# Kernel tuning notes

Hardware: AMD Instinct MI355X
Metric: run time of the kernel (lower is better)

Reference implementation:

```python
import jax, jax.numpy as jnp
import numpy as np

K = 5          # kernel_size
BETA = 15.0    # soft-max temperature
PAD = (K - 1) // 2  # fixed_padding with dilation=1: pad_beg = pad_end = 2


def setup_inputs() -> dict:
    key = jax.random.key(0)
    kx, kw = jax.random.split(key)
    x = jax.random.normal(kx, (16, 8, 256, 256), dtype=jnp.float32)
    weight = jax.random.normal(kw, (8, 8, K, K), dtype=jnp.float32) * 0.1
    return {"x": x, "weight": weight}


def reference(x, weight):
    """Morphological dilation2d with soft-max (logsumexp) reduction.

    Equivalent to: unfold(pad(x)) -> (B,1,C*K*K,L); add weight.view(O,-1);
    logsumexp(beta * .) / beta over the C*K*K axis; reshape to (B,O,H,W).
    Implemented as a streaming logsumexp over the K*K taps to avoid the
    huge unfold intermediate.
    """
    B, C, H, W = x.shape
    O = weight.shape[0]
    xp = jnp.pad(x, ((0, 0), (0, 0), (PAD, PAD), (PAD, PAD)))
    acc = None
    for ki in range(K):
        for kj in range(K):
            xs = xp[:, :, ki:ki + H, kj:kj + W]              # (B,C,H,W)
            w_tap = weight[:, :, ki, kj]                      # (O,C)
            # beta * (w + x), broadcast to (B,O,C,H,W)
            t = BETA * (xs[:, None, :, :, :] + w_tap[None, :, :, None, None])
            lse = jax.nn.logsumexp(t, axis=2)                 # (B,O,H,W)
            acc = lse if acc is None else jnp.logaddexp(acc, lse)
    return acc / BETA
```

## Files before the change

kernel.cpp:

```cpp
#include <hip/hip_runtime.h>
#include <hip/hip_bf16.h>
#include <math.h>

#define KW 5
#define BETA 15.0f
#define MSHIFT 3.0f
#define CIN 8
#define COUT 8
#define HH 256
#define WW 256
#define TW 64
#define THT 8
#define CWp 68
#define CHp 12

typedef float f32x4 __attribute__((ext_vector_type(4)));
typedef short s16x8 __attribute__((ext_vector_type(8)));

static __device__ __forceinline__ unsigned f2bf(float f) {
    unsigned u = __float_as_uint(f);
    return (u + 0x7FFFu + ((u >> 16) & 1u)) >> 16;
}

__global__ void build_afrag(const float* __restrict__ wgt,
                            s16x8* __restrict__ table) {
    int i = blockIdx.x * 64 + threadIdx.x;
    if (i >= 7 * 64) return;
    int g = i >> 6, lane = i & 63;
    int quad = lane >> 4, row = lane & 15;
    int tap = g * 4 + quad;
    s16x8 af;
    #pragma unroll
    for (int j = 0; j < CIN; ++j) {
        float v = 0.0f;
        if (tap < 25 && row < COUT)
            v = __expf(BETA * wgt[(row * CIN + j) * (KW * KW) + tap]);
        af[j] = (short)f2bf(v);
    }
    table[i] = af;
}

__global__ __launch_bounds__(256, 6) void morph_mfma(
    const float* __restrict__ x, const s16x8* __restrict__ table,
    float* __restrict__ out)
{
    __shared__ int4 exs[CHp * CWp];

    const int tid  = threadIdx.x;
    const int lane = tid & 63;
    const int wv   = tid >> 6;
    const int px   = lane & 15;
    const int quad = lane >> 4;

    const int lid = blockIdx.x;
    const int sw  = (lid & 7) * 256 + (lid >> 3);
    const int b   = sw >> 7;
    const int t   = sw & 127;
    const int h0  = (t >> 2) * THT;
    const int w0  = (t & 3) * TW;

    s16x8 afrag[7];
    int   toff[7];
    #pragma unroll
    for (int g = 0; g < 7; ++g) {
        afrag[g] = table[g * 64 + lane];
        int tap = g * 4 + quad;
        int tc  = tap < 25 ? tap : 24;
        toff[g] = (tc / KW) * CWp + (tc % KW);
    }

    for (int s = tid; s < CHp * CWp; s += 256) {
        int r = s / CWp, col = s - r * CWp;
        int gh = h0 + r - 2, gw = w0 + col - 2;
        bool ok = ((unsigned)gh < (unsigned)HH) & ((unsigned)gw < (unsigned)WW);
        unsigned pk[4];
        #pragma unroll
        for (int c2 = 0; c2 < 4; ++c2) {
            float v0 = 0.0f, v1 = 0.0f;
            if (ok) {
                v0 = x[((b * CIN + 2 * c2) * HH + gh) * WW + gw];
                v1 = x[((b * CIN + 2 * c2 + 1) * HH + gh) * WW + gw];
            }
            float2 e = make_float2(__expf(BETA * (v0 - MSHIFT)),
                                   __expf(BETA * (v1 - MSHIFT)));
            __hip_bfloat162 h2 = __float22bfloat162_rn(e);
            pk[c2] = *reinterpret_cast<unsigned*>(&h2);
        }
        int4 p; p.x = pk[0]; p.y = pk[1]; p.z = pk[2]; p.w = pk[3];
        exs[s] = p;
    }
    __syncthreads();

    const float inv_beta = 1.0f / BETA;
    #pragma unroll
    for (int hl = 0; hl < 2; ++hl) {
        const int hh = wv * 2 + hl;
        #pragma unroll
        for (int wb = 0; wb < 4; ++wb) {
            const int base = hh * CWp + wb * 16 + px;
            f32x4 acc0 = {0.0f, 0.0f, 0.0f, 0.0f};
            f32x4 acc1 = {0.0f, 0.0f, 0.0f, 0.0f};
            #pragma unroll
            for (int g = 0; g < 7; ++g) {
                s16x8 bfr = *(const s16x8*)&exs[base + toff[g]];
                if (g & 1)
                    acc1 = __builtin_amdgcn_mfma_f32_16x16x32_bf16(
                               afrag[g], bfr, acc1, 0, 0, 0);
                else
                    acc0 = __builtin_amdgcn_mfma_f32_16x16x32_bf16(
                               afrag[g], bfr, acc0, 0, 0, 0);
            }
            if (quad < 2) {
                #pragma unroll
                for (int r = 0; r < 4; ++r) {
                    int o = quad * 4 + r;
                    out[((b * COUT + o) * HH + h0 + hh) * WW + w0 + wb * 16 + px]
                        = MSHIFT + __logf(acc0[r] + acc1[r]) * inv_beta;
                }
            }
        }
    }
}

extern "C" void kernel_launch(void* const* d_in, const int* in_sizes, int n_in,
                              void* d_out, int out_size, void* d_ws, size_t ws_size,
                              hipStream_t stream) {
    const float* x   = (const float*)d_in[0];
    const float* wgt = (const float*)d_in[1];
    float* out  = (float*)d_out;
    s16x8* tab  = (s16x8*)d_ws;

    const int B = in_sizes[0] / (CIN * HH * WW);
    const int nblk = B * (HH / THT) * (WW / TW);

    build_afrag<<<7, 64, 0, stream>>>(wgt, tab);
    morph_mfma<<<nblk, 256, 0, stream>>>(x, tab, out);
}
```

Before: 99.42 us.

## Give each wave a private LDS halo tile and drop block barrier

Each of the four waves now stages its own 16x8 output tile plus halo (20x12 exp-transformed pixels) into a private LDS region and computes all 8 rows of it, so the block-wide __syncthreads is removed. This lets waves proceed independently, overlapping staging with MFMA work. The cost is redundant halo loads and exp computations between neighbouring waves and slightly more LDS per block.

```diff
diff --git a/kernel.cpp b/kernel.cpp
--- a/kernel.cpp
+++ b/kernel.cpp
@@ -9,10 +9,11 @@
 #define COUT 8
 #define HH 256
 #define WW 256
-#define TW 64
-#define THT 8
-#define CWp 68
-#define CHp 12
+#define TWW 16
+#define TWH 8
+#define WCW 20
+#define WCH 12
+#define WSLOTS (WCW * WCH)
 
 typedef float f32x4 __attribute__((ext_vector_type(4)));
 typedef short s16x8 __attribute__((ext_vector_type(8)));
@@ -44,7 +45,7 @@
     const float* __restrict__ x, const s16x8* __restrict__ table,
     float* __restrict__ out)
 {
-    __shared__ int4 exs[CHp * CWp];
+    __shared__ int4 exs[4 * WSLOTS];
 
     const int tid  = threadIdx.x;
     const int lane = tid & 63;
@@ -56,8 +57,10 @@
     const int sw  = (lid & 7) * 256 + (lid >> 3);
     const int b   = sw >> 7;
     const int t   = sw & 127;
-    const int h0  = (t >> 2) * THT;
-    const int w0  = (t & 3) * TW;
+    const int h0  = (t >> 2) * TWH;
+    const int w0  = (t & 3) * 64 + wv * TWW;
+
+    int4* myex = &exs[wv * WSLOTS];
 
     s16x8 afrag[7];
     int   toff[7];
@@ -66,11 +69,11 @@
         afrag[g] = table[g * 64 + lane];
         int tap = g * 4 + quad;
         int tc  = tap < 25 ? tap : 24;
-        toff[g] = (tc / KW) * CWp + (tc % KW);
+        toff[g] = (tc / KW) * WCW + (tc % KW);
     }
 
-    for (int s = tid; s < CHp * CWp; s += 256) {
-        int r = s / CWp, col = s - r * CWp;
+    for (int s = lane; s < WSLOTS; s += 64) {
+        int r = s / WCW, col = s - r * WCW;
         int gh = h0 + r - 2, gw = w0 + col - 2;
         bool ok = ((unsigned)gh < (unsigned)HH) & ((unsigned)gw < (unsigned)WW);
         unsigned pk[4];
@@ -87,36 +90,31 @@
             pk[c2] = *reinterpret_cast<unsigned*>(&h2);
         }
         int4 p; p.x = pk[0]; p.y = pk[1]; p.z = pk[2]; p.w = pk[3];
-        exs[s] = p;
+        myex[s] = p;
     }
-    __syncthreads();
 
     const float inv_beta = 1.0f / BETA;
     #pragma unroll
-    for (int hl = 0; hl < 2; ++hl) {
-        const int hh = wv * 2 + hl;
+    for (int hl = 0; hl < TWH; ++hl) {
+        const int base = hl * WCW + px;
+        f32x4 acc0 = {0.0f, 0.0f, 0.0f, 0.0f};
+        f32x4 acc1 = {0.0f, 0.0f, 0.0f, 0.0f};
         #pragma unroll
-        for (int wb = 0; wb < 4; ++wb) {
-            const int base = hh * CWp + wb * 16 + px;
-            f32x4 acc0 = {0.0f, 0.0f, 0.0f, 0.0f};
-            f32x4 acc1 = {0.0f, 0.0f, 0.0f, 0.0f};
+        for (int g = 0; g < 7; ++g) {
+            s16x8 bfr = *(const s16x8*)&myex[base + toff[g]];
+            if (g & 1)
+                acc1 = __builtin_amdgcn_mfma_f32_16x16x32_bf16(
+                           afrag[g], bfr, acc1, 0, 0, 0);
+            else
+                acc0 = __builtin_amdgcn_mfma_f32_16x16x32_bf16(
+                           afrag[g], bfr, acc0, 0, 0, 0);
+        }
+        if (quad < 2) {
             #pragma unroll
-            for (int g = 0; g < 7; ++g) {
-                s16x8 bfr = *(const s16x8*)&exs[base + toff[g]];
-                if (g & 1)
-                    acc1 = __builtin_amdgcn_mfma_f32_16x16x32_bf16(
-                               afrag[g], bfr, acc1, 0, 0, 0);
-                else
-                    acc0 = __builtin_amdgcn_mfma_f32_16x16x32_bf16(
-                               afrag[g], bfr, acc0, 0, 0, 0);
-            }
-            if (quad < 2) {
-                #pragma unroll
-                for (int r = 0; r < 4; ++r) {
-                    int o = quad * 4 + r;
-                    out[((b * COUT + o) * HH + h0 + hh) * WW + w0 + wb * 16 + px]
-                        = MSHIFT + __logf(acc0[r] + acc1[r]) * inv_beta;
-                }
+            for (int r = 0; r < 4; ++r) {
+                int o = quad * 4 + r;
+                out[((b * COUT + o) * HH + h0 + hl) * WW + w0 + px]
+                    = MSHIFT + __logf(acc0[r] + acc1[r]) * inv_beta;
             }
         }
     }
@@ -131,8 +129,7 @@
     s16x8* tab  = (s16x8*)d_ws;
 
     const int B = in_sizes[0] / (CIN * HH * WW);
-    const int nblk = B * (HH / THT) * (WW / TW);
-
+    const int nblk = B * (HH / TWH) * (WW / 64);
     build_afrag<<<7, 64, 0, stream>>>(wgt, tab);
     morph_mfma<<<nblk, 256, 0, stream>>>(x, tab, out);
 }
```

After: 98.61 us. About the same (-0.8%).
